# Kernel tuning notes

Measured on AMD Instinct MI355X. Metric: run time of the kernel, lower is better.

Reference implementation:

```python
import math
import jax, jax.numpy as jnp
import numpy as np

B, L, ENC_IN, TFEAT = 32, 1024, 21, 4
DM, EXP = 256, 2
DI = DM * EXP            # 512 d_inner
DST = 64                 # d_state (= configs.d_ff in this repo)
HD = 64                  # headdim
NH = DI // HD            # 8 heads
DC = 4                   # d_conv
NL = 4                   # n_layers
PRED = 192
CO = 21
Q = 64                   # SSD chunk length
DIP = 2 * DI + 2 * DST + NH    # in_proj out dim (z, xBC, dt)
CONVD = DI + 2 * DST           # depthwise-conv channels


def silu(x):
    return x * jax.nn.sigmoid(x)


def positional_embedding(l, d):
    pe = np.zeros((l, d), np.float32)
    pos = np.arange(l, dtype=np.float32)[:, None]
    div = np.exp(np.arange(0, d, 2, dtype=np.float32) * (-math.log(10000.0) / d))
    pe[:, 0::2] = np.sin(pos * div)
    pe[:, 1::2] = np.cos(pos * div)
    return jnp.asarray(pe)


def layernorm(x, g, b):
    m = jnp.mean(x, -1, keepdims=True)
    v = jnp.mean((x - m) ** 2, -1, keepdims=True)
    return (x - m) * jax.lax.rsqrt(v + 1e-5) * g + b


def segsum(x):
    # x: (..., T) -> (..., T, T); out[i,j] = sum_{j<k<=i} x[k], -inf above diagonal
    T = x.shape[-1]
    xx = jnp.broadcast_to(x[..., :, None], (*x.shape, T))
    m1 = jnp.tril(jnp.ones((T, T), bool), -1)
    xs = jnp.cumsum(jnp.where(m1, xx, 0.0), axis=-2)
    m2 = jnp.tril(jnp.ones((T, T), bool), 0)
    return jnp.where(m2, xs, -jnp.inf)


def ssd(X, A, Bm, Cm):
    # chunked SSD (Mamba2). X: (b,l,h,p) = x*dt; A: (b,l,h) = dt*(-exp(A_log)); B,C: (b,l,n)
    b, l, h, p = X.shape
    c = l // Q
    Xc = X.reshape(b, c, Q, h, p)
    Ac = A.reshape(b, c, Q, h).transpose(0, 3, 1, 2)      # (b,h,c,q)
    Bc = Bm.reshape(b, c, Q, -1)
    Cc = Cm.reshape(b, c, Q, -1)
    Acum = jnp.cumsum(Ac, -1)                              # (b,h,c,q)
    Lmat = jnp.exp(segsum(Ac))                             # (b,h,c,q,q)
    Y_diag = jnp.einsum('bcqn,bcsn,bhcqs,bcshp->bcqhp', Cc, Bc, Lmat, Xc)
    decay_states = jnp.exp(Acum[..., -1:] - Acum)          # (b,h,c,q)
    states = jnp.einsum('bcqn,bhcq,bcqhp->bchpn', Bc, decay_states, Xc)
    states = jnp.concatenate([jnp.zeros_like(states[:, :1]), states], axis=1)  # (b,c+1,h,p,n)
    decay_chunk = jnp.exp(segsum(jnp.pad(Acum[..., -1], ((0, 0), (0, 0), (1, 0)))))  # (b,h,c+1,c+1)
    new_states = jnp.einsum('bhzc,bchpn->bzhpn', decay_chunk, states)
    states = new_states[:, :-1]                            # (b,c,h,p,n) entering each chunk
    sdo = jnp.exp(Acum)                                    # (b,h,c,q)
    Y_off = jnp.einsum('bcqn,bchpn,bhcq->bcqhp', Cc, states, sdo)
    return (Y_diag + Y_off).reshape(b, l, h, p)


def mamba2(x, Wi, cw, cb, dtb, Alog, Dp, gw, Wo):
    b, l, _ = x.shape
    zxbcdt = x @ Wi.T                                      # (b,l,DIP)
    z = zxbcdt[..., :DI]
    xBC = zxbcdt[..., DI:DI + CONVD]
    dt = zxbcdt[..., DI + CONVD:]
    # causal depthwise conv (kernel DC) + SiLU
    xp = jnp.pad(xBC, ((0, 0), (DC - 1, 0), (0, 0)))
    xBC = silu(sum(xp[:, k:k + l, :] * cw[:, k] for k in range(DC)) + cb)
    xs = xBC[..., :DI].reshape(b, l, NH, HD)
    Bm = xBC[..., DI:DI + DST]
    Cm = xBC[..., DI + DST:]
    dt = jax.nn.softplus(dt + dtb)                         # (b,l,NH)
    A = -jnp.exp(Alog)                                     # (NH,)
    y = ssd(xs * dt[..., None], dt * A, Bm, Cm) + xs * Dp[:, None]
    y = y.reshape(b, l, DI)
    y = y * silu(z)                                        # gated RMSNorm
    y = y * jax.lax.rsqrt(jnp.mean(y * y, -1, keepdims=True) + 1e-5) * gw
    return y @ Wo.T


def setup_inputs():
    key = jax.random.key(0)
    ks = jax.random.split(key, 16)
    x_enc = jax.random.normal(ks[0], (B, L, ENC_IN), jnp.float32)
    x_mark_enc = jax.random.normal(ks[1], (B, L, TFEAT), jnp.float32)
    x_dec = jax.random.normal(ks[2], (B, 240, ENC_IN), jnp.float32)
    x_mark_dec = jax.random.normal(ks[3], (B, 240, TFEAT), jnp.float32)
    token_w = jax.random.normal(ks[4], (DM, ENC_IN, 3), jnp.float32) * 0.1
    temb_w = jax.random.normal(ks[5], (DM, TFEAT), jnp.float32) * 0.1
    ln_g = jnp.ones((NL, DM), jnp.float32)
    ln_b = jnp.zeros((NL, DM), jnp.float32)
    in_proj_w = jax.random.normal(ks[6], (NL, DIP, DM), jnp.float32) * (DM ** -0.5)
    conv_w = jax.random.normal(ks[7], (NL, CONVD, DC), jnp.float32) * 0.2
    conv_b = jnp.zeros((NL, CONVD), jnp.float32)
    dt_bias = jax.random.normal(ks[8], (NL, NH), jnp.float32) * 0.5
    A_log = jnp.log(jax.random.uniform(ks[9], (NL, NH), jnp.float32, 1.0, 16.0))
    Dskip = jnp.ones((NL, NH), jnp.float32)
    gnorm_w = jnp.ones((NL, DI), jnp.float32)
    out_proj_w = jax.random.normal(ks[10], (NL, DM, DI), jnp.float32) * (DI ** -0.5)
    head_w = jax.random.normal(ks[11], (CO, DM), jnp.float32) * (DM ** -0.5)
    return dict(x_enc=x_enc, x_mark_enc=x_mark_enc, x_dec=x_dec, x_mark_dec=x_mark_dec,
                token_w=token_w, temb_w=temb_w, ln_g=ln_g, ln_b=ln_b,
                in_proj_w=in_proj_w, conv_w=conv_w, conv_b=conv_b, dt_bias=dt_bias,
                A_log=A_log, Dskip=Dskip, gnorm_w=gnorm_w, out_proj_w=out_proj_w,
                head_w=head_w)


def reference(x_enc, x_mark_enc, x_dec, x_mark_dec, token_w, temb_w, ln_g, ln_b,
              in_proj_w, conv_w, conv_b, dt_bias, A_log, Dskip, gnorm_w, out_proj_w, head_w):
    # instance normalization (detached stats)
    mean = jax.lax.stop_gradient(jnp.mean(x_enc, 1, keepdims=True))
    xz = x_enc - mean
    std = jax.lax.stop_gradient(jnp.sqrt(jnp.var(xz, axis=1, keepdims=True) + 1e-5))
    xz = xz / std
    l = xz.shape[1]
    # token embedding: circular-pad Conv1d(enc_in->d_model, k=3)
    xpad = jnp.pad(xz, ((0, 0), (1, 1), (0, 0)), mode='wrap')
    tok = sum(jnp.einsum('blc,dc->bld', xpad[:, k:k + l], token_w[:, :, k]) for k in range(3))
    h = tok + positional_embedding(l, DM)[None] + x_mark_enc @ temb_w.T
    for i in range(NL):
        y = mamba2(h, in_proj_w[i], conv_w[i], conv_b[i], dt_bias[i], A_log[i],
                   Dskip[i], gnorm_w[i], out_proj_w[i])
        h = layernorm(h + y, ln_g[i], ln_b[i])
    out = h @ head_w.T
    out = out * std + mean
    return out[:, -PRED:, :]
```

## Files before the change

kernel.cpp:

```cpp
#include <hip/hip_runtime.h>
#include <hip/hip_bf16.h>


typedef unsigned short ushort_t;
typedef unsigned int uint_t;
typedef __attribute__((ext_vector_type(8))) short short8;
typedef __attribute__((ext_vector_type(4))) float f32x4;
typedef __attribute__((ext_vector_type(4))) ushort_t ushort4_t;

__device__ __forceinline__ float b2f(ushort_t u) {
    uint_t v = ((uint_t)u) << 16;
    return __builtin_bit_cast(float, v);
}
__device__ __forceinline__ ushort_t f2b(float f) {
    uint_t u = __builtin_bit_cast(uint_t, f);
    uint_t r = (u + 0x7FFFu + ((u >> 16) & 1u)) >> 16;
    return (ushort_t)r;
}
__device__ __forceinline__ float silu_f(float x) {
    return x / (1.f + __expf(-x));
}
__device__ __forceinline__ void gl_lds16(const ushort_t* g, ushort_t* l) {
    __builtin_amdgcn_global_load_lds(
        (const __attribute__((address_space(1))) unsigned int*)g,
        (__attribute__((address_space(3))) unsigned int*)l, 16, 0, 0);
}

__global__ __launch_bounds__(256) void cvt_kernel(const float* __restrict__ in,
        ushort_t* __restrict__ out, int n) {
    int i = blockIdx.x * 256 + threadIdx.x;
    if (i < n) out[i] = f2b(in[i]);
}
__global__ __launch_bounds__(256) void cvt_pad_ip(const float* __restrict__ in,
        ushort_t* __restrict__ out) {
    int i = blockIdx.x * 256 + threadIdx.x;
    if (i >= 4 * 1280 * 256) return;
    int layer = i / (1280 * 256);
    int rem = i - layer * 1280 * 256;
    int n = rem >> 8, k = rem & 255;
    out[i] = (n < 1160) ? f2b(in[(size_t)layer * 1160 * 256 + n * 256 + k]) : (ushort_t)0;
}
__global__ __launch_bounds__(256) void cvt_convw(const float* __restrict__ in,
        float* __restrict__ out) {
    int i = blockIdx.x * 256 + threadIdx.x;
    if (i >= 10240) return;
    int layer = i / 2560;
    int rem = i - layer * 2560;
    int k = rem / 640, ch = rem - k * 640;
    out[i] = in[layer * 2560 + ch * 4 + k];
}

__global__ __launch_bounds__(256) void pe_kernel(float* __restrict__ pe) {
    int l = blockIdx.x, d = threadIdx.x;
    float div = __expf((float)(d & ~1) * (-9.210340371976184f / 256.0f));
    float arg = (float)l * div;
    pe[l * 256 + d] = (d & 1) ? cosf(arg) : sinf(arg);
}

__global__ __launch_bounds__(256) void stats_kernel(const float* __restrict__ xe,
        float* __restrict__ meanb, float* __restrict__ stdb, float* __restrict__ rstdb) {
    int bi = blockIdx.x;
    int b = bi / 21, c = bi - b * 21;
    int tid = threadIdx.x;
    float s = 0.f, s2 = 0.f;
    for (int l = tid; l < 1024; l += 256) {
        float v = xe[(b * 1024 + l) * 21 + c];
        s += v; s2 += v * v;
    }
    __shared__ float r1[4], r2[4];
    for (int o = 32; o > 0; o >>= 1) { s += __shfl_down(s, o, 64); s2 += __shfl_down(s2, o, 64); }
    if ((tid & 63) == 0) { r1[tid >> 6] = s; r2[tid >> 6] = s2; }
    __syncthreads();
    if (tid == 0) {
        float S = r1[0] + r1[1] + r1[2] + r1[3];
        float S2 = r2[0] + r2[1] + r2[2] + r2[3];
        float m = S * (1.f / 1024.f);
        float var = S2 * (1.f / 1024.f) - m * m;
        float sd = sqrtf(var + 1e-5f);
        meanb[bi] = m; stdb[bi] = sd; rstdb[bi] = 1.f / sd;
    }
}

__global__ __launch_bounds__(256) void embed3_kernel(const float* __restrict__ xe,
        const float* __restrict__ xm, const float* __restrict__ tokw,
        const float* __restrict__ tembw, const float* __restrict__ pe,
        const float* __restrict__ meanb, const float* __restrict__ rstdb,
        float* __restrict__ h, ushort_t* __restrict__ hbf) {
    int blk = blockIdx.x;
    int b = blk >> 4, t = blk & 15;
    int l0 = t * 64;
    int tid = threadIdx.x;
    __shared__ float xw[66][22];
    __shared__ float xmw[64][4];
    __shared__ float mn[21], rs[21];
    if (tid < 21) { mn[tid] = meanb[b * 21 + tid]; rs[tid] = rstdb[b * 21 + tid]; }
    float twr[63];
    {
        const float* tp = tokw + tid * 63;
        #pragma unroll
        for (int i = 0; i < 63; i++) twr[i] = tp[i];
    }
    float tbr[4];
    #pragma unroll
    for (int k = 0; k < 4; k++) tbr[k] = tembw[tid * 4 + k];
    __syncthreads();
    for (int i = tid; i < 1386; i += 256) {
        int row = i / 21, c = i - row * 21;
        int gl = (l0 - 1 + row + 1024) & 1023;
        xw[row][c] = (xe[(size_t)(b * 1024 + gl) * 21 + c] - mn[c]) * rs[c];
    }
    {
        int row = tid >> 2, c = tid & 3;
        xmw[row][c] = xm[(size_t)(b * 1024 + l0 + row) * 4 + c];
    }
    __syncthreads();
    int d = tid;
    float acc2 = 0.f, acc1 = 0.f;
    for (int r = 0; r < 66; r++) {
        float s0 = 0.f, s1 = 0.f, s2 = 0.f;
        #pragma unroll
        for (int c = 0; c < 21; c++) {
            float xv = xw[r][c];
            s0 += xv * twr[c * 3 + 0];
            s1 += xv * twr[c * 3 + 1];
            s2 += xv * twr[c * 3 + 2];
        }
        if (r >= 2) {
            int li = r - 2;
            float acc = acc2 + s2 + pe[(size_t)(l0 + li) * 256 + d];
            #pragma unroll
            for (int k = 0; k < 4; k++) acc += xmw[li][k] * tbr[k];
            size_t o = (size_t)(b * 1024 + l0 + li) * 256 + d;
            h[o] = acc;
            hbf[o] = f2b(acc);
        }
        acc2 = acc1 + s1;
        acc1 = s0;
    }
}

template<int KDIM>
__device__ __forceinline__ void gemm128_main(const ushort_t* __restrict__ Ab,
        const ushort_t* __restrict__ Wb, ushort_t* sA, ushort_t* sW,
        f32x4 (&acc)[16], int m0, int n0) {
    int tid = threadIdx.x;
    int w = tid >> 6, lane = tid & 63;
    int wm = w >> 1, wn = w & 1;
    int rr = lane & 15, quad = lane >> 4;
    int srow0 = w * 32 + (lane >> 2);
    int skk = (lane & 3) * 8;
    int sl0 = w * 1024 + lane * 8;
    for (int k0 = 0; k0 < KDIM; k0 += 64) {
        __syncthreads();
        #pragma unroll
        for (int p = 0; p < 2; p++) {
            #pragma unroll
            for (int j = 0; j < 2; j++) {
                int row = srow0 + j * 16;
                int koff = k0 + p * 32 + skk;
                gl_lds16(Ab + (size_t)(m0 + row) * KDIM + koff, &sA[p * 4096 + sl0 + j * 512]);
                gl_lds16(Wb + (size_t)(n0 + row) * KDIM + koff, &sW[p * 4096 + sl0 + j * 512]);
            }
        }
        __syncthreads();
        #pragma unroll
        for (int p = 0; p < 2; p++) {
            short8 a[4], b[4];
            #pragma unroll
            for (int i = 0; i < 4; i++)
                a[i] = *(const short8*)&sA[p * 4096 + (wm * 64 + i * 16 + rr) * 32 + quad * 8];
            #pragma unroll
            for (int j = 0; j < 4; j++)
                b[j] = *(const short8*)&sW[p * 4096 + (wn * 64 + j * 16 + rr) * 32 + quad * 8];
            #pragma unroll
            for (int i = 0; i < 4; i++)
                #pragma unroll
                for (int j = 0; j < 4; j++)
                    acc[i * 4 + j] = __builtin_amdgcn_mfma_f32_16x16x32_bf16(a[i], b[j], acc[i * 4 + j], 0, 0, 0);
        }
    }
}

__global__ __launch_bounds__(256) void gemm_ip(const ushort_t* __restrict__ A,
        const ushort_t* __restrict__ W, ushort_t* __restrict__ zbuf,
        ushort_t* __restrict__ xbuf) {
    int blk = blockIdx.x;
    int tm = blk / 10, tn = blk - tm * 10;
    int m0 = tm * 128, n0 = tn * 128;
    __shared__ ushort_t sA[8192], sW[8192];
    f32x4 acc[16];
    #pragma unroll
    for (int i = 0; i < 16; i++) acc[i] = (f32x4){0.f, 0.f, 0.f, 0.f};
    gemm128_main<256>(A, W, sA, sW, acc, m0, n0);
    int lane = threadIdx.x & 63, w = threadIdx.x >> 6;
    int wm = w >> 1, wn = w & 1;
    int rr = lane & 15, quad = lane >> 4;
    #pragma unroll
    for (int i = 0; i < 4; i++) {
        int mrow = m0 + wm * 64 + i * 16 + quad * 4;
        #pragma unroll
        for (int j = 0; j < 4; j++) {
            int n = n0 + wn * 64 + j * 16 + rr;
            #pragma unroll
            for (int r2 = 0; r2 < 4; r2++) {
                ushort_t v = f2b(acc[i * 4 + j][r2]);
                if (n < 512) zbuf[(size_t)(mrow + r2) * 512 + n] = v;
                else if (n < 1160) xbuf[(size_t)(mrow + r2) * 704 + (n - 512)] = v;
            }
        }
    }
}

__global__ __launch_bounds__(256) void gemm_op(const ushort_t* __restrict__ A,
        const ushort_t* __restrict__ W, float* __restrict__ C) {
    int blk = blockIdx.x;
    int tm = blk >> 1, tn = blk & 1;
    int m0 = tm * 128, n0 = tn * 128;
    __shared__ ushort_t sA[8192], sW[8192];
    f32x4 acc[16];
    #pragma unroll
    for (int i = 0; i < 16; i++) acc[i] = (f32x4){0.f, 0.f, 0.f, 0.f};
    gemm128_main<512>(A, W, sA, sW, acc, m0, n0);
    int lane = threadIdx.x & 63, w = threadIdx.x >> 6;
    int wm = w >> 1, wn = w & 1;
    int rr = lane & 15, quad = lane >> 4;
    #pragma unroll
    for (int i = 0; i < 4; i++) {
        int mrow = m0 + wm * 64 + i * 16 + quad * 4;
        #pragma unroll
        for (int j = 0; j < 4; j++) {
            int n = n0 + wn * 64 + j * 16 + rr;
            #pragma unroll
            for (int r2 = 0; r2 < 4; r2++)
                C[(size_t)(mrow + r2) * 256 + n] = acc[i * 4 + j][r2];
        }
    }
}

__global__ __launch_bounds__(256) void conv_kernel(const ushort_t* __restrict__ xbuf,
        const float* __restrict__ cwt, const float* __restrict__ cb,
        const float* __restrict__ dtb, ushort_t* __restrict__ xc,
        float* __restrict__ dts) {
    if (blockIdx.x >= 2560) {
        int r = (blockIdx.x - 2560) * 256 + threadIdx.x;
        short8 dv = *(const short8*)(xbuf + (size_t)r * 704 + 640);
        #pragma unroll
        for (int j = 0; j < 8; j++) {
            float x = b2f(((ushort_t*)&dv)[j]) + dtb[j];
            dts[(size_t)r * 8 + j] = (x > 20.f) ? x : log1pf(__expf(x));
        }
        return;
    }
    int idx = blockIdx.x * 256 + threadIdx.x;
    int g = idx % 80;
    int rt = idx / 80;
    int ch0 = g * 8;
    int b = rt >> 8;
    int l0 = (rt & 255) << 2;
    float wgt[4][8];
    #pragma unroll
    for (int k = 0; k < 4; k++) {
        float4 w0 = *(const float4*)(cwt + k * 640 + ch0);
        float4 w1 = *(const float4*)(cwt + k * 640 + ch0 + 4);
        wgt[k][0] = w0.x; wgt[k][1] = w0.y; wgt[k][2] = w0.z; wgt[k][3] = w0.w;
        wgt[k][4] = w1.x; wgt[k][5] = w1.y; wgt[k][6] = w1.z; wgt[k][7] = w1.w;
    }
    float bias[8];
    {
        float4 b0 = *(const float4*)(cb + ch0);
        float4 b1 = *(const float4*)(cb + ch0 + 4);
        bias[0] = b0.x; bias[1] = b0.y; bias[2] = b0.z; bias[3] = b0.w;
        bias[4] = b1.x; bias[5] = b1.y; bias[6] = b1.z; bias[7] = b1.w;
    }
    short8 xr[7];
    const ushort_t* base = xbuf + (size_t)(b * 1024 + l0) * 704 + ch0;
    #pragma unroll
    for (int i = 0; i < 7; i++) {
        int ll = l0 - 3 + i;
        if (ll >= 0) xr[i] = *(const short8*)(base + (ptrdiff_t)(i - 3) * 704);
        else         xr[i] = (short8){0, 0, 0, 0, 0, 0, 0, 0};
    }
    #pragma unroll
    for (int lo = 0; lo < 4; lo++) {
        float acc[8];
        #pragma unroll
        for (int j = 0; j < 8; j++) acc[j] = bias[j];
        #pragma unroll
        for (int k = 0; k < 4; k++) {
            #pragma unroll
            for (int j = 0; j < 8; j++)
                acc[j] += b2f(((ushort_t*)&xr[lo + k])[j]) * wgt[k][j];
        }
        short8 o;
        #pragma unroll
        for (int j = 0; j < 8; j++) ((ushort_t*)&o)[j] = f2b(silu_f(acc[j]));
        *(short8*)(xc + (size_t)(b * 1024 + l0 + lo) * 640 + ch0) = o;
    }
}

__global__ __launch_bounds__(256) void ssd_stateA4(const ushort_t* __restrict__ xc,
        const float* __restrict__ dts, const float* __restrict__ alog,
        float* __restrict__ stbuf, float* __restrict__ acbuf) {
    int idx = blockIdx.x;
    int bh = idx >> 2, grp = idx & 3;
    int b = bh >> 3, h = bh & 7;
    float Ah = -__expf(alog[h]);
    int tid = threadIdx.x;
    int q = tid >> 2, pb = (tid & 3) * 16;
    int w = tid >> 6, lane = tid & 63;
    int rr = lane & 15, quad = lane >> 4, qb = w * 16;

    __shared__ ushort_t Bt[64][72], Xt[64][72];
    __shared__ float dec_s[64];
    __shared__ float ad_sh;

    float T[4][4];
    #pragma unroll
    for (int t = 0; t < 4; t++)
        #pragma unroll
        for (int r2 = 0; r2 < 4; r2++) T[t][r2] = 0.f;

    for (int c4 = 0; c4 < 4; c4++) {
        int chunk = grp * 4 + c4;
        int l0 = chunk * 64;
        size_t cidx = (size_t)bh * 16 + chunk;
        const ushort_t* xrow = xc + (size_t)(b * 1024 + l0 + q) * 640;
        ushort_t bv[16], xv[16];
        *(short8*)&bv[0] = *(const short8*)(xrow + 512 + pb);
        *(short8*)&bv[8] = *(const short8*)(xrow + 512 + pb + 8);
        *(short8*)&xv[0] = *(const short8*)(xrow + h * 64 + pb);
        *(short8*)&xv[8] = *(const short8*)(xrow + h * 64 + pb + 8);
        #pragma unroll
        for (int j = 0; j < 16; j++) Xt[pb + j][q] = xv[j];

        if (tid < 64) {
            float d = dts[(size_t)(b * 1024 + l0 + tid) * 8 + h];
            float a = d * Ah;
            #pragma unroll
            for (int off = 1; off < 64; off <<= 1) {
                float t = __shfl_up(a, off, 64);
                if (tid >= off) a += t;
            }
            acbuf[cidx * 64 + tid] = a;
            float tot = __shfl(a, 63, 64);
            dec_s[tid] = __expf(tot - a) * d;
            if (tid == 0) ad_sh = __expf(tot);
        }
        __syncthreads();
        {
            float dq = dec_s[q];
            #pragma unroll
            for (int j = 0; j < 16; j++) Bt[pb + j][q] = f2b(b2f(bv[j]) * dq);
        }
        __syncthreads();

        f32x4 acc[4];
        #pragma unroll
        for (int t = 0; t < 4; t++) acc[t] = (f32x4){0.f, 0.f, 0.f, 0.f};
        #pragma unroll
        for (int ks = 0; ks < 2; ks++) {
            short8 a = *(const short8*)(&Bt[qb + rr][ks * 32 + quad * 8]);
            #pragma unroll
            for (int t = 0; t < 4; t++) {
                short8 bb = *(const short8*)(&Xt[t * 16 + rr][ks * 32 + quad * 8]);
                acc[t] = __builtin_amdgcn_mfma_f32_16x16x32_bf16(a, bb, acc[t], 0, 0, 0);
            }
        }
        {
            float ad = ad_sh;
            #pragma unroll
            for (int t = 0; t < 4; t++)
                #pragma unroll
                for (int r2 = 0; r2 < 4; r2++)
                    T[t][r2] = ad * T[t][r2] + acc[t][r2];
        }
        __syncthreads();
    }
    float* sb = stbuf + (size_t)idx * 4096;
    #pragma unroll
    for (int t = 0; t < 4; t++) {
        int p = t * 16 + rr;
        #pragma unroll
        for (int r2 = 0; r2 < 4; r2++)
            sb[(qb + quad * 4 + r2) * 64 + p] = T[t][r2];
    }
}

__global__ __launch_bounds__(256) void ssd_scan(const float* __restrict__ stbuf,
        const float* __restrict__ acbuf, float* __restrict__ gst) {
    int bh = blockIdx.x >> 2, sl = blockIdx.x & 3;
    int tid = threadIdx.x;
    size_t boff = (size_t)sl * 1024 + tid * 4;
    float4 S = make_float4(0.f, 0.f, 0.f, 0.f);
    for (int g = 0; g < 4; g++) {
        *(float4*)(gst + (size_t)(bh * 4 + g) * 4096 + boff) = S;
        float Ag = 1.f;
        #pragma unroll
        for (int c = 0; c < 4; c++)
            Ag *= __expf(acbuf[((size_t)bh * 16 + g * 4 + c) * 64 + 63]);
        float4 v = *(const float4*)(stbuf + (size_t)(bh * 4 + g) * 4096 + boff);
        S.x = Ag * S.x + v.x; S.y = Ag * S.y + v.y;
        S.z = Ag * S.z + v.z; S.w = Ag * S.w + v.w;
    }
}

__global__ __launch_bounds__(256) void ssd_outBC4(const ushort_t* __restrict__ xc,
        const float* __restrict__ dts, const float* __restrict__ acbuf,
        const float* __restrict__ dsk, const float* __restrict__ gst,
        ushort_t* __restrict__ ybuf) {
    int idx = blockIdx.x;
    int bh = idx >> 2, grp = idx & 3;
    int b = bh >> 3, h = bh & 7;
    float Dh = dsk[h];
    int tid = threadIdx.x;
    int q = tid >> 2, pb = (tid & 3) * 16;
    int w = tid >> 6, lane = tid & 63;
    int rr = lane & 15, quad = lane >> 4, qb = w * 16;

    __shared__ ushort_t Cs[64][72], Bs[64][72], Xt[64][72], Gs[64][72], Shi[64][72], Slo[64][72];
    __shared__ float acum_s[64], dtq_s[64], ea_s[64], dec_s[64];
    __shared__ float ad_sh;

    float S[4][4];
    {
        const float* s0 = gst + (size_t)idx * 4096;
        #pragma unroll
        for (int t = 0; t < 4; t++) {
            int p = t * 16 + rr;
            #pragma unroll
            for (int r2 = 0; r2 < 4; r2++)
                S[t][r2] = s0[(qb + quad * 4 + r2) * 64 + p];
        }
    }

    for (int c4 = 0; c4 < 4; c4++) {
        int chunk = grp * 4 + c4;
        int l0 = chunk * 64;
        size_t cidx = (size_t)bh * 16 + chunk;
        const ushort_t* xrow = xc + (size_t)(b * 1024 + l0 + q) * 640;
        *(short8*)&Bs[q][pb]     = *(const short8*)(xrow + 512 + pb);
        *(short8*)&Bs[q][pb + 8] = *(const short8*)(xrow + 512 + pb + 8);
        *(short8*)&Cs[q][pb]     = *(const short8*)(xrow + 576 + pb);
        *(short8*)&Cs[q][pb + 8] = *(const short8*)(xrow + 576 + pb + 8);
        ushort_t xv[16];
        *(short8*)&xv[0] = *(const short8*)(xrow + h * 64 + pb);
        *(short8*)&xv[8] = *(const short8*)(xrow + h * 64 + pb + 8);
        #pragma unroll
        for (int j = 0; j < 16; j++) Xt[pb + j][q] = xv[j];
        if (tid < 64) {
            float a = acbuf[cidx * 64 + tid];
            acum_s[tid] = a;
            ea_s[tid] = __expf(a);
            float d = dts[(size_t)(b * 1024 + l0 + tid) * 8 + h];
            dtq_s[tid] = d;
            float tot = acbuf[cidx * 64 + 63];
            dec_s[tid] = __expf(tot - a) * d;
            if (tid == 0) ad_sh = __expf(tot);
        }
        #pragma unroll
        for (int t = 0; t < 4; t++) {
            int p = t * 16 + rr;
            #pragma unroll
            for (int r2 = 0; r2 < 4; r2++) {
                float s = S[t][r2];
                ushort_t hi = f2b(s);
                Shi[p][qb + quad * 4 + r2] = hi;
                Slo[p][qb + quad * 4 + r2] = f2b(s - b2f(hi));
            }
        }
        __syncthreads();

        {
            f32x4 g[4];
            #pragma unroll
            for (int t = 0; t < 4; t++) g[t] = (f32x4){0.f, 0.f, 0.f, 0.f};
            #pragma unroll
            for (int ks = 0; ks < 2; ks++) {
                short8 a = *(const short8*)(&Cs[qb + rr][ks * 32 + quad * 8]);
                #pragma unroll
                for (int t = 0; t < 4; t++) {
                    short8 bb = *(const short8*)(&Bs[t * 16 + rr][ks * 32 + quad * 8]);
                    g[t] = __builtin_amdgcn_mfma_f32_16x16x32_bf16(a, bb, g[t], 0, 0, 0);
                }
            }
            #pragma unroll
            for (int t = 0; t < 4; t++) {
                int s = t * 16 + rr;
                float as = acum_s[s], dss = dtq_s[s];
                #pragma unroll
                for (int r2 = 0; r2 < 4; r2++) {
                    int qq = qb + quad * 4 + r2;
                    float v = (s <= qq) ? g[t][r2] * __expf(acum_s[qq] - as) * dss : 0.f;
                    Gs[qq][s] = f2b(v);
                }
            }
        }
        __syncthreads();

        f32x4 aD[4], aO[4];
        #pragma unroll
        for (int t = 0; t < 4; t++) { aD[t] = (f32x4){0.f,0.f,0.f,0.f}; aO[t] = (f32x4){0.f,0.f,0.f,0.f}; }
        #pragma unroll
        for (int ks = 0; ks < 2; ks++) {
            short8 ga = *(const short8*)(&Gs[qb + rr][ks * 32 + quad * 8]);
            short8 ca = *(const short8*)(&Cs[qb + rr][ks * 32 + quad * 8]);
            #pragma unroll
            for (int t = 0; t < 4; t++) {
                short8 xb = *(const short8*)(&Xt[t * 16 + rr][ks * 32 + quad * 8]);
                short8 sh = *(const short8*)(&Shi[t * 16 + rr][ks * 32 + quad * 8]);
                short8 sl = *(const short8*)(&Slo[t * 16 + rr][ks * 32 + quad * 8]);
                aD[t] = __builtin_amdgcn_mfma_f32_16x16x32_bf16(ga, xb, aD[t], 0, 0, 0);
                aO[t] = __builtin_amdgcn_mfma_f32_16x16x32_bf16(ca, sh, aO[t], 0, 0, 0);
                aO[t] = __builtin_amdgcn_mfma_f32_16x16x32_bf16(ca, sl, aO[t], 0, 0, 0);
            }
        }
        #pragma unroll
        for (int t = 0; t < 4; t++) {
            int p = t * 16 + rr;
            #pragma unroll
            for (int r2 = 0; r2 < 4; r2++) {
                int qq = qb + quad * 4 + r2;
                float y = aD[t][r2] + ea_s[qq] * aO[t][r2] + Dh * b2f(Xt[p][qq]);
                ybuf[(size_t)(b * 1024 + l0 + qq) * 512 + h * 64 + p] = f2b(y);
            }
        }
        __syncthreads();

        {
            float dq = dec_s[q];
            #pragma unroll
            for (int j = 0; j < 16; j++)
                Gs[pb + j][q] = f2b(b2f(Bs[q][pb + j]) * dq);
        }
        __syncthreads();

        {
            f32x4 acc[4];
            #pragma unroll
            for (int t = 0; t < 4; t++) acc[t] = (f32x4){0.f, 0.f, 0.f, 0.f};
            #pragma unroll
            for (int ks = 0; ks < 2; ks++) {
                short8 a = *(const short8*)(&Gs[qb + rr][ks * 32 + quad * 8]);
                #pragma unroll
                for (int t = 0; t < 4; t++) {
                    short8 bb = *(const short8*)(&Xt[t * 16 + rr][ks * 32 + quad * 8]);
                    acc[t] = __builtin_amdgcn_mfma_f32_16x16x32_bf16(a, bb, acc[t], 0, 0, 0);
                }
            }
            float ad = ad_sh;
            #pragma unroll
            for (int t = 0; t < 4; t++)
                #pragma unroll
                for (int r2 = 0; r2 < 4; r2++)
                    S[t][r2] = ad * S[t][r2] + acc[t][r2];
        }
        __syncthreads();
    }
}

__global__ __launch_bounds__(256) void gate_kernel(const ushort_t* __restrict__ zbuf,
        ushort_t* __restrict__ ybuf, const float* __restrict__ gw) {
    int row = blockIdx.x * 4 + (threadIdx.x >> 6);
    int lane = threadIdx.x & 63;
    size_t base = (size_t)row * 512 + lane * 8;
    short8 zv = *(const short8*)(zbuf + base);
    short8 yv = *(const short8*)(ybuf + base);
    float v[8];
    float ss = 0.f;
    #pragma unroll
    for (int j = 0; j < 8; j++) {
        v[j] = b2f(((ushort_t*)&yv)[j]) * silu_f(b2f(((ushort_t*)&zv)[j]));
        ss += v[j] * v[j];
    }
    #pragma unroll
    for (int o = 1; o < 64; o <<= 1) ss += __shfl_xor(ss, o, 64);
    float rms = rsqrtf(ss * (1.f / 512.f) + 1e-5f);
    float4 g0 = *(const float4*)(gw + lane * 8);
    float4 g1 = *(const float4*)(gw + lane * 8 + 4);
    float gv[8] = {g0.x, g0.y, g0.z, g0.w, g1.x, g1.y, g1.z, g1.w};
    short8 o;
    #pragma unroll
    for (int j = 0; j < 8; j++) ((ushort_t*)&o)[j] = f2b(v[j] * rms * gv[j]);
    *(short8*)(ybuf + base) = o;
}

__global__ __launch_bounds__(256) void resln_kernel(float* __restrict__ h,
        ushort_t* __restrict__ hbf, const float* __restrict__ yp,
        const float* __restrict__ g, const float* __restrict__ bb) {
    int row = blockIdx.x * 4 + (threadIdx.x >> 6);
    int lane = threadIdx.x & 63;
    size_t base = (size_t)row * 256 + lane * 4;
    float4 hv = *(const float4*)(h + base);
    float4 yv = *(const float4*)(yp + base);
    float x[4] = {hv.x + yv.x, hv.y + yv.y, hv.z + yv.z, hv.w + yv.w};
    float s = 0.f, s2 = 0.f;
    #pragma unroll
    for (int j = 0; j < 4; j++) { s += x[j]; s2 += x[j] * x[j]; }
    #pragma unroll
    for (int o = 1; o < 64; o <<= 1) { s += __shfl_xor(s, o, 64); s2 += __shfl_xor(s2, o, 64); }
    float mu = s * (1.f / 256.f);
    float var = s2 * (1.f / 256.f) - mu * mu;
    float rstd = rsqrtf(var + 1e-5f);
    float4 gv = *(const float4*)(g + lane * 4);
    float4 bv = *(const float4*)(bb + lane * 4);
    float gr[4] = {gv.x, gv.y, gv.z, gv.w};
    float br[4] = {bv.x, bv.y, bv.z, bv.w};
    float4 ho;
    ushort4_t bo;
    #pragma unroll
    for (int j = 0; j < 4; j++) {
        float o = (x[j] - mu) * rstd * gr[j] + br[j];
        ((float*)&ho)[j] = o;
        bo[j] = f2b(o);
    }
    *(float4*)(h + base) = ho;
    *(ushort4_t*)(hbf + base) = bo;
}

__global__ __launch_bounds__(256) void head_kernel(const float* __restrict__ h,
        const float* __restrict__ hw, const float* __restrict__ stdb,
        const float* __restrict__ meanb, float* __restrict__ out) {
    int blk = blockIdx.x;
    int b = blk / 192, t = blk - b * 192;
    int l = 832 + t;
    int tid = threadIdx.x;
    __shared__ float hr[256];
    hr[tid] = h[(size_t)(b * 1024 + l) * 256 + tid];
    __syncthreads();
    if (tid < 21) {
        float acc = 0.f;
        for (int k = 0; k < 256; k++) acc += hr[k] * hw[tid * 256 + k];
        out[(size_t)blk * 21 + tid] = acc * stdb[b * 21 + tid] + meanb[b * 21 + tid];
    }
}

extern "C" void kernel_launch(void* const* d_in, const int* in_sizes, int n_in,
                              void* d_out, int out_size, void* d_ws, size_t ws_size,
                              hipStream_t stream) {
    const float* x_enc  = (const float*)d_in[0];
    const float* x_mark = (const float*)d_in[1];
    const float* tokw   = (const float*)d_in[4];
    const float* tembw  = (const float*)d_in[5];
    const float* ln_g   = (const float*)d_in[6];
    const float* ln_b   = (const float*)d_in[7];
    const float* ipw    = (const float*)d_in[8];
    const float* cw     = (const float*)d_in[9];
    const float* cb     = (const float*)d_in[10];
    const float* dtb    = (const float*)d_in[11];
    const float* alog   = (const float*)d_in[12];
    const float* dsk    = (const float*)d_in[13];
    const float* gw     = (const float*)d_in[14];
    const float* opw    = (const float*)d_in[15];
    const float* hw     = (const float*)d_in[16];
    float* out = (float*)d_out;

    char* w = (char*)d_ws;
    size_t off = 0;
    auto alloc = [&](size_t bytes) -> void* {
        void* p = w + off;
        off += (bytes + 255) & ~(size_t)255;
        return p;
    };
    float* meanb  = (float*)alloc(672 * 4);
    float* stdb   = (float*)alloc(672 * 4);
    float* rstdb  = (float*)alloc(672 * 4);
    float* dts    = (float*)alloc((size_t)262144 * 4);
    float* pebuf  = (float*)alloc((size_t)262144 * 4);
    float* cwt    = (float*)alloc((size_t)10240 * 4);
    float* hbuf   = (float*)alloc((size_t)8388608 * 4);
    ushort_t* hbf = (ushort_t*)alloc((size_t)8388608 * 2);
    ushort_t* zbuf= (ushort_t*)alloc((size_t)32768 * 512 * 2);
    ushort_t* xc  = (ushort_t*)alloc((size_t)32768 * 640 * 2);
    char* R       = (char*)alloc((size_t)71303168);
    ushort_t* ybuf= (ushort_t*)alloc((size_t)32768 * 512 * 2);
    ushort_t* wipb= (ushort_t*)alloc((size_t)4 * 1280 * 256 * 2);
    ushort_t* wopb= (ushort_t*)alloc((size_t)4 * 256 * 512 * 2);
    ushort_t* xbuf = (ushort_t*)R;
    float* stbuf   = (float*)R;
    float* acbuf   = (float*)(R + 67108864);
    float* yproj   = (float*)xc;
    float* gst     = (float*)hbf;
    (void)ws_size; (void)in_sizes; (void)n_in; (void)out_size;

    stats_kernel<<<672, 256, 0, stream>>>(x_enc, meanb, stdb, rstdb);
    pe_kernel<<<1024, 256, 0, stream>>>(pebuf);
    cvt_pad_ip<<<5120, 256, 0, stream>>>(ipw, wipb);
    cvt_kernel<<<2048, 256, 0, stream>>>(opw, wopb, 524288);
    cvt_convw<<<40, 256, 0, stream>>>(cw, cwt);
    embed3_kernel<<<512, 256, 0, stream>>>(x_enc, x_mark, tokw, tembw, pebuf,
                                           meanb, rstdb, hbuf, hbf);

    for (int layer = 0; layer < 4; layer++) {
        gemm_ip<<<2560, 256, 0, stream>>>(hbf, wipb + (size_t)layer * 1280 * 256,
                                          zbuf, xbuf);
        conv_kernel<<<2688, 256, 0, stream>>>(xbuf, cwt + layer * 2560,
                                              cb + layer * 640, dtb + layer * 8,
                                              xc, dts);
        ssd_stateA4<<<1024, 256, 0, stream>>>(xc, dts, alog + layer * 8, stbuf, acbuf);
        ssd_scan<<<1024, 256, 0, stream>>>(stbuf, acbuf, gst);
        ssd_outBC4<<<1024, 256, 0, stream>>>(xc, dts, acbuf, dsk + layer * 8,
                                             gst, ybuf);
        gate_kernel<<<8192, 256, 0, stream>>>(zbuf, ybuf, gw + layer * 512);
        gemm_op<<<512, 256, 0, stream>>>(ybuf, wopb + (size_t)layer * 256 * 512, yproj);
        resln_kernel<<<8192, 256, 0, stream>>>(hbuf, hbf, yproj,
                                               ln_g + layer * 256, ln_b + layer * 256);
    }

    head_kernel<<<6144, 256, 0, stream>>>(hbuf, hw, stdb, meanb, out);
}
```

Baseline: 886.1 us.

## Fuse gating RMSNorm, out-projection GEMM, residual and LayerNorm into one kernel

Replaces the gate, out-projection GEMM and residual-LayerNorm kernels with a single kernel. It computes y*silu(z) on the fly while staging the A tile, accumulates the per-row sum of squares, and applies the RMS scale after the GEMM. The gnorm weight is folded into the bf16 out-proj weights at conversion time. The LayerNorm then runs on the accumulator tile with the full 256-column row held in the block. This removes two elementwise passes and the fp32 yproj round-trip through memory. In exchange the GEMM uses 64-row tiles with global-to-register loads for A and no double buffering.

```diff
diff --git a/kernel.cpp b/kernel.cpp
--- a/kernel.cpp
+++ b/kernel.cpp
@@ -26,11 +26,6 @@
         (__attribute__((address_space(3))) unsigned int*)l, 16, 0, 0);
 }
 
-__global__ __launch_bounds__(256) void cvt_kernel(const float* __restrict__ in,
-        ushort_t* __restrict__ out, int n) {
-    int i = blockIdx.x * 256 + threadIdx.x;
-    if (i < n) out[i] = f2b(in[i]);
-}
 __global__ __launch_bounds__(256) void cvt_pad_ip(const float* __restrict__ in,
         ushort_t* __restrict__ out) {
     int i = blockIdx.x * 256 + threadIdx.x;
@@ -39,6 +34,13 @@
     int rem = i - layer * 1280 * 256;
     int n = rem >> 8, k = rem & 255;
     out[i] = (n < 1160) ? f2b(in[(size_t)layer * 1160 * 256 + n * 256 + k]) : (ushort_t)0;
+}
+__global__ __launch_bounds__(256) void cvt_wop(const float* __restrict__ in,
+        const float* __restrict__ gw, ushort_t* __restrict__ out) {
+    int i = blockIdx.x * 256 + threadIdx.x;
+    int layer = i >> 17;
+    int c = i & 511;
+    out[i] = f2b(in[i] * gw[layer * 512 + c]);
 }
 __global__ __launch_bounds__(256) void cvt_convw(const float* __restrict__ in,
         float* __restrict__ out) {
@@ -211,28 +213,140 @@
     }
 }
 
-__global__ __launch_bounds__(256) void gemm_op(const ushort_t* __restrict__ A,
-        const ushort_t* __restrict__ W, float* __restrict__ C) {
-    int blk = blockIdx.x;
-    int tm = blk >> 1, tn = blk & 1;
-    int m0 = tm * 128, n0 = tn * 128;
-    __shared__ ushort_t sA[8192], sW[8192];
-    f32x4 acc[16];
-    #pragma unroll
-    for (int i = 0; i < 16; i++) acc[i] = (f32x4){0.f, 0.f, 0.f, 0.f};
-    gemm128_main<512>(A, W, sA, sW, acc, m0, n0);
-    int lane = threadIdx.x & 63, w = threadIdx.x >> 6;
+__global__ __launch_bounds__(256) void gemm_og(const ushort_t* __restrict__ Yb,
+        const ushort_t* __restrict__ Zb, const ushort_t* __restrict__ Wb,
+        float* __restrict__ h, ushort_t* __restrict__ hbf,
+        const float* __restrict__ lng, const float* __restrict__ lnb) {
+    int m0 = blockIdx.x * 64;
+    int tid = threadIdx.x;
+    int w = tid >> 6, lane = tid & 63;
     int wm = w >> 1, wn = w & 1;
     int rr = lane & 15, quad = lane >> 4;
-    #pragma unroll
-    for (int i = 0; i < 4; i++) {
-        int mrow = m0 + wm * 64 + i * 16 + quad * 4;
-        #pragma unroll
-        for (int j = 0; j < 4; j++) {
-            int n = n0 + wn * 64 + j * 16 + rr;
-            #pragma unroll
-            for (int r2 = 0; r2 < 4; r2++)
-                C[(size_t)(mrow + r2) * 256 + n] = acc[i * 4 + j][r2];
+    __shared__ ushort_t sA[4096];
+    __shared__ ushort_t sW[16384];
+    __shared__ float gssq[64];
+    __shared__ float rsum[64][2], rssq[64][2];
+
+    int arow = tid >> 2;
+    int akq = (tid & 3) * 16;
+    const ushort_t* yrow = Yb + (size_t)(m0 + arow) * 512 + akq;
+    const ushort_t* zrow = Zb + (size_t)(m0 + arow) * 512 + akq;
+    ushort_t* adst = &sA[((tid & 3) >> 1) * 2048 + arow * 32 + (tid & 1) * 16];
+
+    f32x4 acc[2][8];
+    #pragma unroll
+    for (int i = 0; i < 2; i++)
+        #pragma unroll
+        for (int j = 0; j < 8; j++) acc[i][j] = (f32x4){0.f, 0.f, 0.f, 0.f};
+    float ssqr = 0.f;
+
+    short8 y0 = *(const short8*)(yrow);
+    short8 y1 = *(const short8*)(yrow + 8);
+    short8 z0 = *(const short8*)(zrow);
+    short8 z1 = *(const short8*)(zrow + 8);
+
+    for (int k0 = 0; k0 < 512; k0 += 64) {
+        __syncthreads();
+        short8 ga, gb;
+        #pragma unroll
+        for (int jj = 0; jj < 8; jj++) {
+            float g = b2f(((ushort_t*)&y0)[jj]) * silu_f(b2f(((ushort_t*)&z0)[jj]));
+            ssqr += g * g;
+            ((ushort_t*)&ga)[jj] = f2b(g);
+        }
+        #pragma unroll
+        for (int jj = 0; jj < 8; jj++) {
+            float g = b2f(((ushort_t*)&y1)[jj]) * silu_f(b2f(((ushort_t*)&z1)[jj]));
+            ssqr += g * g;
+            ((ushort_t*)&gb)[jj] = f2b(g);
+        }
+        *(short8*)adst = ga;
+        *(short8*)(adst + 8) = gb;
+        if (k0 + 64 < 512) {
+            y0 = *(const short8*)(yrow + k0 + 64);
+            y1 = *(const short8*)(yrow + k0 + 72);
+            z0 = *(const short8*)(zrow + k0 + 64);
+            z1 = *(const short8*)(zrow + k0 + 72);
+        }
+        #pragma unroll
+        for (int p = 0; p < 2; p++) {
+            #pragma unroll
+            for (int j = 0; j < 4; j++)
+                gl_lds16(Wb + (size_t)(w * 64 + j * 16 + (lane >> 2)) * 512
+                             + k0 + p * 32 + (lane & 3) * 8,
+                         &sW[p * 8192 + w * 2048 + j * 512 + lane * 8]);
+        }
+        __syncthreads();
+        #pragma unroll
+        for (int p = 0; p < 2; p++) {
+            short8 a[2], b[8];
+            #pragma unroll
+            for (int i = 0; i < 2; i++)
+                a[i] = *(const short8*)&sA[p * 2048 + (wm * 32 + i * 16 + rr) * 32 + quad * 8];
+            #pragma unroll
+            for (int j = 0; j < 8; j++)
+                b[j] = *(const short8*)&sW[p * 8192 + (wn * 128 + j * 16 + rr) * 32 + quad * 8];
+            #pragma unroll
+            for (int i = 0; i < 2; i++)
+                #pragma unroll
+                for (int j = 0; j < 8; j++)
+                    acc[i][j] = __builtin_amdgcn_mfma_f32_16x16x32_bf16(a[i], b[j], acc[i][j], 0, 0, 0);
+        }
+    }
+
+    ssqr += __shfl_xor(ssqr, 1, 64);
+    ssqr += __shfl_xor(ssqr, 2, 64);
+    if ((tid & 3) == 0) gssq[arow] = ssqr;
+    __syncthreads();
+
+    float gl[8], bl[8];
+    #pragma unroll
+    for (int j = 0; j < 8; j++) {
+        int col = wn * 128 + j * 16 + rr;
+        gl[j] = lng[col]; bl[j] = lnb[col];
+    }
+    #pragma unroll
+    for (int i = 0; i < 2; i++) {
+        #pragma unroll
+        for (int r2 = 0; r2 < 4; r2++) {
+            int rowl = wm * 32 + i * 16 + quad * 4 + r2;
+            float rmsv = rsqrtf(gssq[rowl] * (1.f / 512.f) + 1e-5f);
+            size_t gbase = (size_t)(m0 + rowl) * 256;
+            float s = 0.f, s2 = 0.f;
+            #pragma unroll
+            for (int j = 0; j < 8; j++) {
+                int col = wn * 128 + j * 16 + rr;
+                float xv = h[gbase + col] + acc[i][j][r2] * rmsv;
+                acc[i][j][r2] = xv;
+                s += xv; s2 += xv * xv;
+            }
+            #pragma unroll
+            for (int o = 1; o < 16; o <<= 1) {
+                s += __shfl_xor(s, o, 64);
+                s2 += __shfl_xor(s2, o, 64);
+            }
+            if (rr == 0) { rsum[rowl][wn] = s; rssq[rowl][wn] = s2; }
+        }
+    }
+    __syncthreads();
+    #pragma unroll
+    for (int i = 0; i < 2; i++) {
+        #pragma unroll
+        for (int r2 = 0; r2 < 4; r2++) {
+            int rowl = wm * 32 + i * 16 + quad * 4 + r2;
+            float S = rsum[rowl][0] + rsum[rowl][1];
+            float S2 = rssq[rowl][0] + rssq[rowl][1];
+            float mu = S * (1.f / 256.f);
+            float var = S2 * (1.f / 256.f) - mu * mu;
+            float rstd = rsqrtf(var + 1e-5f);
+            size_t gbase = (size_t)(m0 + rowl) * 256;
+            #pragma unroll
+            for (int j = 0; j < 8; j++) {
+                int col = wn * 128 + j * 16 + rr;
+                float o = (acc[i][j][r2] - mu) * rstd * gl[j] + bl[j];
+                h[gbase + col] = o;
+                hbf[gbase + col] = f2b(o);
+            }
         }
     }
 }
@@ -556,65 +670,6 @@
         }
         __syncthreads();
     }
-}
-
-__global__ __launch_bounds__(256) void gate_kernel(const ushort_t* __restrict__ zbuf,
-        ushort_t* __restrict__ ybuf, const float* __restrict__ gw) {
-    int row = blockIdx.x * 4 + (threadIdx.x >> 6);
-    int lane = threadIdx.x & 63;
-    size_t base = (size_t)row * 512 + lane * 8;
-    short8 zv = *(const short8*)(zbuf + base);
-    short8 yv = *(const short8*)(ybuf + base);
-    float v[8];
-    float ss = 0.f;
-    #pragma unroll
-    for (int j = 0; j < 8; j++) {
-        v[j] = b2f(((ushort_t*)&yv)[j]) * silu_f(b2f(((ushort_t*)&zv)[j]));
-        ss += v[j] * v[j];
-    }
-    #pragma unroll
-    for (int o = 1; o < 64; o <<= 1) ss += __shfl_xor(ss, o, 64);
-    float rms = rsqrtf(ss * (1.f / 512.f) + 1e-5f);
-    float4 g0 = *(const float4*)(gw + lane * 8);
-    float4 g1 = *(const float4*)(gw + lane * 8 + 4);
-    float gv[8] = {g0.x, g0.y, g0.z, g0.w, g1.x, g1.y, g1.z, g1.w};
-    short8 o;
-    #pragma unroll
-    for (int j = 0; j < 8; j++) ((ushort_t*)&o)[j] = f2b(v[j] * rms * gv[j]);
-    *(short8*)(ybuf + base) = o;
-}
-
-__global__ __launch_bounds__(256) void resln_kernel(float* __restrict__ h,
-        ushort_t* __restrict__ hbf, const float* __restrict__ yp,
-        const float* __restrict__ g, const float* __restrict__ bb) {
-    int row = blockIdx.x * 4 + (threadIdx.x >> 6);
-    int lane = threadIdx.x & 63;
-    size_t base = (size_t)row * 256 + lane * 4;
-    float4 hv = *(const float4*)(h + base);
-    float4 yv = *(const float4*)(yp + base);
-    float x[4] = {hv.x + yv.x, hv.y + yv.y, hv.z + yv.z, hv.w + yv.w};
-    float s = 0.f, s2 = 0.f;
-    #pragma unroll
-    for (int j = 0; j < 4; j++) { s += x[j]; s2 += x[j] * x[j]; }
-    #pragma unroll
-    for (int o = 1; o < 64; o <<= 1) { s += __shfl_xor(s, o, 64); s2 += __shfl_xor(s2, o, 64); }
-    float mu = s * (1.f / 256.f);
-    float var = s2 * (1.f / 256.f) - mu * mu;
-    float rstd = rsqrtf(var + 1e-5f);
-    float4 gv = *(const float4*)(g + lane * 4);
-    float4 bv = *(const float4*)(bb + lane * 4);
-    float gr[4] = {gv.x, gv.y, gv.z, gv.w};
-    float br[4] = {bv.x, bv.y, bv.z, bv.w};
-    float4 ho;
-    ushort4_t bo;
-    #pragma unroll
-    for (int j = 0; j < 4; j++) {
-        float o = (x[j] - mu) * rstd * gr[j] + br[j];
-        ((float*)&ho)[j] = o;
-        bo[j] = f2b(o);
-    }
-    *(float4*)(h + base) = ho;
-    *(ushort4_t*)(hbf + base) = bo;
 }
 
 __global__ __launch_bounds__(256) void head_kernel(const float* __restrict__ h,
@@ -678,14 +733,13 @@
     ushort_t* xbuf = (ushort_t*)R;
     float* stbuf   = (float*)R;
     float* acbuf   = (float*)(R + 67108864);
-    float* yproj   = (float*)xc;
     float* gst     = (float*)hbf;
     (void)ws_size; (void)in_sizes; (void)n_in; (void)out_size;
 
     stats_kernel<<<672, 256, 0, stream>>>(x_enc, meanb, stdb, rstdb);
     pe_kernel<<<1024, 256, 0, stream>>>(pebuf);
     cvt_pad_ip<<<5120, 256, 0, stream>>>(ipw, wipb);
-    cvt_kernel<<<2048, 256, 0, stream>>>(opw, wopb, 524288);
+    cvt_wop<<<2048, 256, 0, stream>>>(opw, gw, wopb);
     cvt_convw<<<40, 256, 0, stream>>>(cw, cwt);
     embed3_kernel<<<512, 256, 0, stream>>>(x_enc, x_mark, tokw, tembw, pebuf,
                                            meanb, rstdb, hbuf, hbf);
@@ -700,10 +754,10 @@
         ssd_scan<<<1024, 256, 0, stream>>>(stbuf, acbuf, gst);
         ssd_outBC4<<<1024, 256, 0, stream>>>(xc, dts, acbuf, dsk + layer * 8,
                                              gst, ybuf);
-        gate_kernel<<<8192, 256, 0, stream>>>(zbuf, ybuf, gw + layer * 512);
-        gemm_op<<<512, 256, 0, stream>>>(ybuf, wopb + (size_t)layer * 256 * 512, yproj);
-        resln_kernel<<<8192, 256, 0, stream>>>(hbuf, hbf, yproj,
-                                               ln_g + layer * 256, ln_b + layer * 256);
+        gemm_og<<<512, 256, 0, stream>>>(ybuf, zbuf,
+                                         wopb + (size_t)layer * 256 * 512,
+                                         hbuf, hbf,
+                                         ln_g + layer * 256, ln_b + layer * 256);
     }
 
     head_kernel<<<6144, 256, 0, stream>>>(hbuf, hw, stdb, meanb, out);
```

Result: faster. 797.4 us (-10.0%).
